# Optimization experiments

Measured on AMD Instinct MI355X. Metric: run time of the kernel, lower is better.

## Reference

```python
import jax, jax.numpy as jnp
import numpy as np
from jax import lax

B, T, D, H = 4, 2048, 1024, 8
DK = D // H        # head qk dim (expand_k=1.0) = 128
DV = 2 * D // H    # head v dim (expand_v=2.0) = 256
C = 64             # retention chunk size


def setup_inputs() -> dict:
    key = jax.random.key(0)
    ks = jax.random.split(key, 7)
    s = 0.02
    return {
        "x": jax.random.normal(ks[0], (B, T, D), jnp.float32),
        "Wq": jax.random.normal(ks[1], (D, H * DK), jnp.float32) * s,
        "Wk": jax.random.normal(ks[2], (D, H * DK), jnp.float32) * s,
        "Wv": jax.random.normal(ks[3], (D, H * DV), jnp.float32) * s,
        "Wg": jax.random.normal(ks[4], (D, H * DV), jnp.float32) * s,
        "Wo": jax.random.normal(ks[5], (H * DV, D), jnp.float32) * s,
        "norm_w": jnp.ones((DV,), jnp.float32),
    }


def _rope(x):
    # x: [B,T,H,DK]; GPT-NeoX style (non-interleaved) rotary, base 10000
    half = DK // 2
    inv = 1.0 / (10000.0 ** (jnp.arange(0, DK, 2, dtype=jnp.float32) / DK))
    f = jnp.arange(T, dtype=jnp.float32)[:, None] * inv[None, :]  # [T, half]
    cos = jnp.cos(f)[None, :, None, :]
    sin = jnp.sin(f)[None, :, None, :]
    x1, x2 = x[..., :half], x[..., half:]
    return jnp.concatenate([x1 * cos - x2 * sin, x2 * cos + x1 * sin], axis=-1)


def _retention(q, k, v):
    # chunked decay-gated linear attention (RetNet retention)
    # q,k: [B,T,H,DK], v: [B,T,H,DV]; recurrence S_t = g*S_{t-1} + k_t^T v_t, o_t = q_t S_t
    N = T // C
    gamma = 1.0 - 2.0 ** (-5.0 - jnp.arange(H, dtype=jnp.float32))  # [H] per-head decay
    i = jnp.arange(C, dtype=jnp.float32)
    expo = i[:, None] - i[None, :]                                   # [C,C]
    M = jnp.where(expo >= 0, gamma[:, None, None] ** expo[None], 0.0)  # [H,C,C] intra-chunk decay mask
    dec_q = gamma[:, None] ** (i + 1.0)        # [H,C] decay of state seen by q_i
    dec_k = gamma[:, None] ** (C - 1.0 - i)    # [H,C] decay of k_j into end-of-chunk state
    gC = gamma ** C

    def to_chunks(t):
        return t.reshape(B, N, C, H, -1).transpose(1, 0, 3, 2, 4)  # [N,B,H,C,d]

    qs, kcs, vcs = to_chunks(q), to_chunks(k), to_chunks(v)

    def step(S, inp):
        qc, kc, vc = inp  # [B,H,C,DK],[B,H,C,DK],[B,H,C,DV]
        attn = jnp.einsum('bhid,bhjd->bhij', qc, kc) * M[None]
        o_intra = jnp.einsum('bhij,bhje->bhie', attn, vc)
        o_inter = jnp.einsum('bhid,bhde->bhie', qc, S) * dec_q[None, :, :, None]
        kv = jnp.einsum('bhjd,bhje->bhde', kc * dec_k[None, :, :, None], vc)
        S_new = gC[None, :, None, None] * S + kv
        return S_new, o_intra + o_inter

    S0 = jnp.zeros((B, H, DK, DV), q.dtype)
    _, os_ = lax.scan(step, S0, (qs, kcs, vcs))  # os_: [N,B,H,C,DV]
    return os_.transpose(1, 0, 3, 2, 4).reshape(B, T, H, DV)


def reference(x, Wq, Wk, Wv, Wg, Wo, norm_w):
    q = (x @ Wq).reshape(B, T, H, DK)
    k = (x @ Wk).reshape(B, T, H, DK)
    v = (x @ Wv).reshape(B, T, H, DV)
    g = (x @ Wg).reshape(B, T, H, DV)
    q, k = _rope(q), _rope(k)
    q = q * (DK ** -0.5)
    o = _retention(q, k, v)
    # fused per-head RMSNorm + swish output gate (FusedRMSNormSwishGate)
    rms = jnp.sqrt(jnp.mean(o * o, axis=-1, keepdims=True) + 1e-5)
    o = (o / rms) * norm_w
    o = o * g * jax.nn.sigmoid(g)
    return o.reshape(B, T, H * DV) @ Wo
```

## Files before the change

### kernel.cpp

```cpp
#include <hip/hip_runtime.h>
#include <hip/hip_bf16.h>
#include <cstdint>
#include <cstddef>

using f32x4 = __attribute__((ext_vector_type(4))) float;
using s16x8 = __attribute__((ext_vector_type(8))) short;
using s16x4 = __attribute__((ext_vector_type(4))) short;

#define DEVINL __device__ __forceinline__

static constexpr int T_LEN  = 2048;
static constexpr int MROWS  = 8192;
static constexpr int NCHUNK = 32;

DEVINL float bf2f(short s){
  unsigned u = ((unsigned)(unsigned short)s) << 16;
  return __builtin_bit_cast(float, u);
}
DEVINL short f2bf(float f){
  unsigned u = __builtin_bit_cast(unsigned, f);
  u = (u + 0x7fffu + ((u >> 16) & 1u)) >> 16;
  return (short)(unsigned short)u;
}

#define GLOAD16(gp, lp) \
  __builtin_amdgcn_global_load_lds((__attribute__((address_space(1))) void*)(gp), \
                                   (__attribute__((address_space(3))) void*)(lp), 16, 0, 0)

#define MFMA16(a, b, c) __builtin_amdgcn_mfma_f32_16x16x32_bf16((a), (b), (c), 0, 0, 0)

__global__ __launch_bounds__(256) void cvt_f32_bf16(const float* __restrict__ in,
                                                    short* __restrict__ out, int n4){
  int i = blockIdx.x * 256 + threadIdx.x;
  if (i >= n4) return;
  float4 v = ((const float4*)in)[i];
  short4 o;
  o.x = f2bf(v.x); o.y = f2bf(v.y); o.z = f2bf(v.z); o.w = f2bf(v.w);
  ((short4*)out)[i] = o;
}

__global__ __launch_bounds__(256) void tr_w(const float* __restrict__ in,
                                            short* __restrict__ out, int R, int C){
  __shared__ float tile[32][33];
  int c0 = blockIdx.x * 32, r0 = blockIdx.y * 32;
  int tx = threadIdx.x, ty = threadIdx.y;
  #pragma unroll
  for (int i = 0; i < 4; ++i){
    int r = ty + i * 8;
    tile[r][tx] = in[(size_t)(r0 + r) * C + c0 + tx];
  }
  __syncthreads();
  #pragma unroll
  for (int i = 0; i < 4; ++i){
    int c = ty + i * 8;
    out[(size_t)(c0 + c) * R + r0 + tx] = f2bf(tile[tx][c]);
  }
}

__global__ __launch_bounds__(256) void tr_k_decay(const short* __restrict__ in,
                                                  short* __restrict__ out){
  __shared__ float tile[32][33];
  int c0 = blockIdx.x * 32, r0 = blockIdx.y * 32;
  int tx = threadIdx.x, ty = threadIdx.y;
  #pragma unroll
  for (int i = 0; i < 4; ++i){
    int r = ty + i * 8;
    tile[r][tx] = bf2f(in[(size_t)(r0 + r) * 1024 + c0 + tx]);
  }
  __syncthreads();
  #pragma unroll
  for (int i = 0; i < 4; ++i){
    int c  = c0 + ty + i * 8;
    int h  = c >> 7;
    float lg = log2f(1.0f - exp2f(-(float)(5 + h)));
    int srow = r0 + tx;
    int j = srow & 63;
    float dec = exp2f((float)(63 - j) * lg);
    out[(size_t)c * MROWS + srow] = f2bf(tile[tx][ty + i * 8] * dec);
  }
}

__global__ __launch_bounds__(256) void rope_table(float* __restrict__ tab){
  int i = blockIdx.x * 256 + threadIdx.x;
  int t = i >> 6, d = i & 63;
  float inv = exp2f(-(float)d * (13.287712379549449f / 64.0f));
  float f = (float)t * inv;
  float s, c;
  sincosf(f, &s, &c);
  tab[2 * i]     = c;
  tab[2 * i + 1] = s;
}

__global__ __launch_bounds__(256) void rope_inplace(short* __restrict__ qk,
                                                    const float* __restrict__ tab,
                                                    float scale, int bake){
  int idx = blockIdx.x * 256 + threadIdx.x;
  int bt  = idx >> 9, rem = idx & 511;
  int h   = rem >> 6, d = rem & 63;
  int t   = bt & (T_LEN - 1);
  float2 cs = ((const float2*)tab)[t * 64 + d];
  float mult = scale;
  if (bake){
    float lg = log2f(1.0f - exp2f(-(float)(5 + h)));
    mult *= exp2f((float)((t & 63) + 1) * lg);
  }
  size_t base = (size_t)bt * 1024 + h * 128 + d;
  float x1 = bf2f(qk[base]), x2 = bf2f(qk[base + 64]);
  qk[base]      = f2bf((x1 * cs.x - x2 * cs.y) * mult);
  qk[base + 64] = f2bf((x2 * cs.x + x1 * cs.y) * mult);
}

DEVINL void stage_half(const short* __restrict__ src, int ldk, int t, int half,
                       short* lbase, int wave, int lane){
  const int sr = lane >> 3;
  const int gc = ((lane & 7) ^ sr) * 8;
  const size_t k0 = (size_t)t * 64;
  #pragma unroll
  for (int c = 0; c < 2; ++c){
    int r0 = half * 128 + c * 64;
    GLOAD16(src + (size_t)(r0 + wave * 8 + sr) * ldk + k0 + gc,
            lbase + (r0 + wave * 8) * 64);
  }
}

DEVINL s16x8 frag64(const short* buf, int row, int ks, int lhi){
  int ch = (ks * 4 + lhi) ^ (row & 7);
  return *(const s16x8*)&buf[row * 64 + ch * 8];
}

template<int MODE>
__global__ __launch_bounds__(512, 2) void gemm256(const short* __restrict__ A,
                                                  const short* __restrict__ Bt,
                                                  void* __restrict__ o0, void* __restrict__ o1,
                                                  void* __restrict__ o2, void* __restrict__ o3,
                                                  int K, int nt){
  __shared__ alignas(16) short LBUF[65536];
  const int tid = threadIdx.x, wave = tid >> 6, lane = tid & 63;
  const int l15 = lane & 15, lhi = lane >> 4;
  const int wm = (wave >> 2) * 128, wn = (wave & 3) * 64;
  const int cpx = gridDim.x >> 3;
  const int swz = (blockIdx.x & 7) * cpx + (blockIdx.x >> 3);
  const int m0 = (swz & 31) * 256, n0 = (swz >> 5) * 256;
  const short* Ag = A + (size_t)m0 * K;
  const short* Bg = Bt + (size_t)n0 * K;
  f32x4 acc[8][4] = {};
  stage_half(Ag, K, 0, 0, LBUF,                 wave, lane);
  stage_half(Ag, K, 0, 1, LBUF,                 wave, lane);
  stage_half(Bg, K, 0, 0, LBUF + 32768,         wave, lane);
  stage_half(Bg, K, 0, 1, LBUF + 32768,         wave, lane);
  stage_half(Bg, K, 1, 0, LBUF + 32768 + 16384, wave, lane);
  stage_half(Bg, K, 1, 1, LBUF + 32768 + 16384, wave, lane);
  asm volatile("s_waitcnt vmcnt(4)" ::: "memory");
  __builtin_amdgcn_sched_barrier(0);
  __builtin_amdgcn_s_barrier();
  for (int t = 0; t < nt; ++t){
    short* Ab = LBUF + (t & 1) * 16384;
    short* Bb = LBUF + 32768 + (t & 1) * 16384;
    s16x8 bfr[2][4];
    #pragma unroll
    for (int q = 0; q < 4; ++q){
      if (q == 0){
        #pragma unroll
        for (int ks = 0; ks < 2; ++ks)
          #pragma unroll
          for (int nf = 0; nf < 4; ++nf)
            bfr[ks][nf] = frag64(Bb, wn + nf * 16 + l15, ks, lhi);
      }
      s16x8 af[2][2];
      #pragma unroll
      for (int i = 0; i < 2; ++i)
        #pragma unroll
        for (int ks = 0; ks < 2; ++ks)
          af[i][ks] = frag64(Ab, wm + (2 * q + i) * 16 + l15, ks, lhi);
      if (q == 0 && t + 1 < nt) stage_half(Ag, K, t + 1, 0, LBUF + ((t + 1) & 1) * 16384, wave, lane);
      if (q == 1 && t + 1 < nt) stage_half(Ag, K, t + 1, 1, LBUF + ((t + 1) & 1) * 16384, wave, lane);
      if (q == 2 && t + 2 < nt) stage_half(Bg, K, t + 2, 0, LBUF + 32768 + (t & 1) * 16384, wave, lane);
      if (q == 3 && t + 2 < nt) stage_half(Bg, K, t + 2, 1, LBUF + 32768 + (t & 1) * 16384, wave, lane);
      __builtin_amdgcn_sched_barrier(0);
      __builtin_amdgcn_s_barrier();
      asm volatile("s_waitcnt lgkmcnt(0)" ::: "memory");
      __builtin_amdgcn_sched_barrier(0);
      __builtin_amdgcn_s_setprio(1);
      #pragma unroll
      for (int i = 0; i < 2; ++i)
        #pragma unroll
        for (int nf = 0; nf < 4; ++nf)
          #pragma unroll
          for (int ks = 0; ks < 2; ++ks)
            acc[2 * q + i][nf] = MFMA16(af[i][ks], bfr[ks][nf], acc[2 * q + i][nf]);
      __builtin_amdgcn_s_setprio(0);
      if (q == 3){
        if (t < nt - 2)       asm volatile("s_waitcnt vmcnt(4)" ::: "memory");
        else if (t == nt - 2) asm volatile("s_waitcnt vmcnt(0)" ::: "memory");
        __builtin_amdgcn_sched_barrier(0);
      }
      __builtin_amdgcn_s_barrier();
    }
  }
  if (MODE == 2){
    float* dst = (float*)o0;
    #pragma unroll
    for (int mf = 0; mf < 8; ++mf){
      int rb = m0 + wm + mf * 16 + 4 * lhi;
      #pragma unroll
      for (int nf = 0; nf < 4; ++nf){
        int col = n0 + wn + nf * 16 + l15;
        #pragma unroll
        for (int r = 0; r < 4; ++r) dst[(size_t)(rb + r) * 1024 + col] = acc[mf][nf][r];
      }
    }
  } else {
    if (n0 < 2048){
      short* dst = (short*)(n0 < 1024 ? o0 : o1);
      int cb = (n0 & 1023) + wn;
      #pragma unroll
      for (int mf = 0; mf < 8; ++mf){
        int rb = m0 + wm + mf * 16 + 4 * lhi;
        #pragma unroll
        for (int nf = 0; nf < 4; ++nf){
          int col = cb + nf * 16 + l15;
          #pragma unroll
          for (int r = 0; r < 4; ++r) dst[(size_t)(rb + r) * 1024 + col] = f2bf(acc[mf][nf][r]);
        }
      }
    } else if (n0 < 4096){
      short* dst = (short*)o2;
      #pragma unroll
      for (int mf = 0; mf < 8; ++mf){
        int rb = m0 + wm + mf * 16 + 4 * lhi;
        #pragma unroll
        for (int nf = 0; nf < 4; ++nf){
          int e = (n0 - 2048) + wn + nf * 16 + l15;
          s16x4 pk;
          #pragma unroll
          for (int r = 0; r < 4; ++r) pk[r] = f2bf(acc[mf][nf][r]);
          *(s16x4*)&dst[(size_t)e * MROWS + rb] = pk;
        }
      }
    } else {
      short* dst = (short*)o3;
      int cb = (n0 - 4096) + wn;
      #pragma unroll
      for (int mf = 0; mf < 8; ++mf){
        int rb = m0 + wm + mf * 16 + 4 * lhi;
        #pragma unroll
        for (int nf = 0; nf < 4; ++nf){
          int col = cb + nf * 16 + l15;
          #pragma unroll
          for (int r = 0; r < 4; ++r) dst[(size_t)(rb + r) * 2048 + col] = f2bf(acc[mf][nf][r]);
        }
      }
    }
  }
}

__global__ __launch_bounds__(256) void ret_scan(const short* __restrict__ kT,
                                                const short* __restrict__ vT,
                                                short* __restrict__ ST){
  __shared__ alignas(16) short kbuf[3][4096];
  __shared__ alignas(16) short vbuf[3][4096];
  const int tid = threadIdx.x, wave = tid >> 6, lane = tid & 63;
  const int db = blockIdx.x & 1, eb = blockIdx.x >> 1;
  const int h = blockIdx.y, b = blockIdx.z;
  const int d0 = db * 64, e0 = eb * 64;
  const float lg = log2f(1.0f - exp2f(-(float)(5 + h)));
  const float gC = exp2f(64.0f * lg);
  f32x4 Sacc[4] = {};
  const int srow = wave * 8 + (lane >> 3);
  const int sc   = lane & 7;

  auto STAGE = [&](int n, int buf){
    size_t rowbase = (size_t)(b * T_LEN + n * 64);
    #pragma unroll
    for (int c = 0; c < 2; ++c){
      int r = c * 32 + srow;
      int gc = sc ^ (r & 7);
      GLOAD16(kT + (size_t)(h * 128 + d0 + r) * MROWS + rowbase + gc * 8,
              &kbuf[buf][c * 2048 + wave * 512]);
    }
    #pragma unroll
    for (int c = 0; c < 2; ++c){
      int r = c * 32 + srow;
      int gc = sc ^ (r & 7);
      GLOAD16(vT + (size_t)(h * 256 + e0 + r) * MROWS + rowbase + gc * 8,
              &vbuf[buf][c * 2048 + wave * 512]);
    }
  };

  STAGE(0, 0);
  STAGE(1, 1);
  for (int n = 0; n < NCHUNK; ++n){
    const int buf = n % 3;
    if (n + 2 < NCHUNK) STAGE(n + 2, (n + 2) % 3);
    if (n > 0){
      size_t stb = (((size_t)n * 4 + b) * 8 + h) * 32768;
      int dbase = d0 + 16 * wave + 4 * (lane >> 4);
      #pragma unroll
      for (int nf = 0; nf < 4; ++nf){
        int e = e0 + nf * 16 + (lane & 15);
        s16x4 pk;
        #pragma unroll
        for (int r = 0; r < 4; ++r) pk[r] = f2bf(Sacc[nf][r]);
        *(s16x4*)&ST[stb + (size_t)e * 128 + dbase] = pk;
      }
    }
    if (n == 0)       asm volatile("s_waitcnt vmcnt(8)"  ::: "memory");
    else if (n < 30)  asm volatile("s_waitcnt vmcnt(12)" ::: "memory");
    else if (n == 30) asm volatile("s_waitcnt vmcnt(8)"  ::: "memory");
    else              asm volatile("s_waitcnt vmcnt(4)"  ::: "memory");
    __builtin_amdgcn_s_barrier();
    __builtin_amdgcn_sched_barrier(0);
    #pragma unroll
    for (int nf = 0; nf < 4; ++nf)
      #pragma unroll
      for (int r = 0; r < 4; ++r) Sacc[nf][r] *= gC;
    #pragma unroll
    for (int ks = 0; ks < 2; ++ks){
      int d = 16 * wave + (lane & 15);
      int chA = (ks * 4 + (lane >> 4)) ^ (d & 7);
      s16x8 af = *(const s16x8*)&kbuf[buf][d * 64 + chA * 8];
      #pragma unroll
      for (int nf = 0; nf < 4; ++nf){
        int e = nf * 16 + (lane & 15);
        int chB = (ks * 4 + (lane >> 4)) ^ (e & 7);
        s16x8 bv = *(const s16x8*)&vbuf[buf][e * 64 + chB * 8];
        Sacc[nf] = MFMA16(af, bv, Sacc[nf]);
      }
    }
    __builtin_amdgcn_s_barrier();
    __builtin_amdgcn_sched_barrier(0);
  }
}

__global__ __launch_bounds__(256, 2) void ret_fused(const short* __restrict__ q,
                                                    const short* __restrict__ k,
                                                    const short* __restrict__ vT,
                                                    const short* __restrict__ ST,
                                                    const short* __restrict__ g,
                                                    const float* __restrict__ nw,
                                                    short* __restrict__ y){
  __shared__ alignas(16) short GS[16384];
  __shared__ alignas(16) float SS[256];
  __shared__ alignas(16) short XS[16896];
  short* PS = XS;
  short* YT = XS;
  const int tid = threadIdx.x, wave = tid >> 6, lane = tid & 63;
  const int l15 = lane & 15, lhi = lane >> 4;
  const int n = blockIdx.x, h = blockIdx.y, b = blockIdx.z;
  const size_t rowbase = (size_t)(b * T_LEN + n * 64);
  {
    int row = wave * 2 + (lane >> 5), sc32 = lane & 31;
    #pragma unroll
    for (int c = 0; c < 8; ++c){
      int r = c * 8 + row;
      GLOAD16(g + (rowbase + r) * 2048 + h * 256 + sc32 * 8, &GS[c * 2048 + wave * 512]);
    }
  }
  s16x8 Qf[4][4];
  #pragma unroll
  for (int rf = 0; rf < 4; ++rf)
    #pragma unroll
    for (int ks = 0; ks < 4; ++ks)
      Qf[rf][ks] = *(const s16x8*)&q[(rowbase + rf * 16 + l15) * 1024 + h * 128 + ks * 32 + lhi * 8];
  s16x8 Kf[4];
  #pragma unroll
  for (int ks = 0; ks < 4; ++ks)
    Kf[ks] = *(const s16x8*)&k[(rowbase + wave * 16 + l15) * 1024 + h * 128 + ks * 32 + lhi * 8];
  f32x4 accP[4] = {};
  #pragma unroll
  for (int ks = 0; ks < 4; ++ks)
    #pragma unroll
    for (int nf = 0; nf < 4; ++nf)
      accP[nf] = MFMA16(Kf[ks], Qf[nf][ks], accP[nf]);
  const float lg = log2f(1.0f - exp2f(-(float)(5 + h)));
  {
    int jb = wave * 16 + 4 * lhi;
    float dj[4];
    #pragma unroll
    for (int r = 0; r < 4; ++r) dj[r] = exp2f(-(float)(jb + r + 1) * lg);
    #pragma unroll
    for (int nf = 0; nf < 4; ++nf){
      int i = nf * 16 + l15;
      s16x4 pk;
      #pragma unroll
      for (int r = 0; r < 4; ++r)
        pk[r] = f2bf((i >= jb + r) ? accP[nf][r] * dj[r] : 0.0f);
      *(s16x4*)&PS[i * 72 + jb] = pk;
    }
  }
  f32x4 acc[4][4] = {};
  if (n){
    size_t stb = (((size_t)n * 4 + b) * 8 + h) * 32768;
    #pragma unroll
    for (int ks = 0; ks < 4; ++ks){
      s16x8 Sf[4];
      #pragma unroll
      for (int nf = 0; nf < 4; ++nf){
        int e = wave * 64 + nf * 16 + l15;
        Sf[nf] = *(const s16x8*)&ST[stb + (size_t)e * 128 + ks * 32 + lhi * 8];
      }
      #pragma unroll
      for (int mf = 0; mf < 4; ++mf)
        #pragma unroll
        for (int nf = 0; nf < 4; ++nf)
          acc[mf][nf] = MFMA16(Qf[mf][ks], Sf[nf], acc[mf][nf]);
    }
  }
  s16x8 Vf[2][4];
  #pragma unroll
  for (int ks2 = 0; ks2 < 2; ++ks2)
    #pragma unroll
    for (int nf = 0; nf < 4; ++nf){
      int e = wave * 64 + nf * 16 + l15;
      Vf[ks2][nf] = *(const s16x8*)&vT[(size_t)(h * 256 + e) * MROWS + rowbase + ks2 * 32 + lhi * 8];
    }
  __syncthreads();
  #pragma unroll
  for (int ks2 = 0; ks2 < 2; ++ks2){
    s16x8 Pf[4];
    #pragma unroll
    for (int mf = 0; mf < 4; ++mf)
      Pf[mf] = *(const s16x8*)&PS[(mf * 16 + l15) * 72 + ks2 * 32 + lhi * 8];
    #pragma unroll
    for (int mf = 0; mf < 4; ++mf)
      #pragma unroll
      for (int nf = 0; nf < 4; ++nf)
        acc[mf][nf] = MFMA16(Pf[mf], Vf[ks2][nf], acc[mf][nf]);
  }
  float ssp[4][4];
  #pragma unroll
  for (int mf = 0; mf < 4; ++mf)
    #pragma unroll
    for (int r = 0; r < 4; ++r){
      float s = 0.f;
      #pragma unroll
      for (int nf = 0; nf < 4; ++nf) s += acc[mf][nf][r] * acc[mf][nf][r];
      #pragma unroll
      for (int off = 8; off >= 1; off >>= 1) s += __shfl_xor(s, off, 64);
      ssp[mf][r] = s;
    }
  if (l15 == 0){
    #pragma unroll
    for (int mf = 0; mf < 4; ++mf)
      #pragma unroll
      for (int r = 0; r < 4; ++r){
        int row = mf * 16 + 4 * lhi + r;
        SS[row * 4 + wave] = ssp[mf][r];
      }
  }
  __syncthreads();
  #pragma unroll
  for (int mf = 0; mf < 4; ++mf){
    float rr[4];
    #pragma unroll
    for (int r = 0; r < 4; ++r){
      int row = mf * 16 + 4 * lhi + r;
      f32x4 s4 = *(const f32x4*)&SS[row * 4];
      float tot = s4[0] + s4[1] + s4[2] + s4[3];
      rr[r] = __builtin_amdgcn_rsqf(tot * (1.0f / 256.0f) + 1e-5f);
    }
    #pragma unroll
    for (int nf = 0; nf < 4; ++nf){
      int e = wave * 64 + nf * 16 + l15;
      float nwe = nw[e];
      #pragma unroll
      for (int r = 0; r < 4; ++r){
        int row = mf * 16 + 4 * lhi + r;
        float gf = bf2f(GS[row * 256 + e]);
        float sig = __builtin_amdgcn_rcpf(1.0f + exp2f(gf * -1.4426950408889634f));
        YT[row * 264 + e] = f2bf(acc[mf][nf][r] * rr[r] * nwe * gf * sig);
      }
    }
  }
  __syncthreads();
  #pragma unroll
  for (int it = 0; it < 8; ++it){
    int flat = it * 2048 + tid * 8;
    int row = flat >> 8, e = flat & 255;
    s16x8 v = *(const s16x8*)&YT[row * 264 + e];
    *(s16x8*)&y[(rowbase + row) * 2048 + h * 256 + e] = v;
  }
}

extern "C" void kernel_launch(void* const* d_in, const int* in_sizes, int n_in,
                              void* d_out, int out_size, void* d_ws, size_t ws_size,
                              hipStream_t stream){
  const float* x  = (const float*)d_in[0];
  const float* Wq = (const float*)d_in[1];
  const float* Wk = (const float*)d_in[2];
  const float* Wv = (const float*)d_in[3];
  const float* Wg = (const float*)d_in[4];
  const float* Wo = (const float*)d_in[5];
  const float* nw = (const float*)d_in[6];
  float* out = (float*)d_out;

  char* w = (char*)d_ws;
  short* xb  = (short*)w;               w += (size_t)8192 * 1024 * 2;
  short* WT  = (short*)w;               w += (size_t)6144 * 1024 * 2;
  short* kTt = (short*)w;               w += (size_t)1024 * 8192 * 2;
  short* qb  = (short*)w;               w += (size_t)8192 * 1024 * 2;
  short* kb  = (short*)w;               w += (size_t)8192 * 1024 * 2;
  short* vT  = (short*)w;               w += (size_t)2048 * 8192 * 2;
  short* gb  = (short*)w;               w += (size_t)8192 * 2048 * 2;
  short* STb = (short*)w;               w += (size_t)32 * 4 * 8 * 32768 * 2;
  short* WoT = (short*)w;               w += (size_t)1024 * 2048 * 2;
  short* yb  = (short*)d_ws;
  float* tab = (float*)STb;

  cvt_f32_bf16<<<8192, 256, 0, stream>>>(x, xb, 8192 * 1024 / 4);
  dim3 tb(32, 8);
  tr_w<<<dim3(32, 32), tb, 0, stream>>>(Wq, WT,                       1024, 1024);
  tr_w<<<dim3(32, 32), tb, 0, stream>>>(Wk, WT + (size_t)1024 * 1024, 1024, 1024);
  tr_w<<<dim3(64, 32), tb, 0, stream>>>(Wv, WT + (size_t)2048 * 1024, 1024, 2048);
  tr_w<<<dim3(64, 32), tb, 0, stream>>>(Wg, WT + (size_t)4096 * 1024, 1024, 2048);
  tr_w<<<dim3(32, 64), tb, 0, stream>>>(Wo, WoT,                      2048, 1024);
  rope_table<<<512, 256, 0, stream>>>(tab);

  gemm256<3><<<768, 512, 0, stream>>>(xb, WT, qb, kb, vT, gb, 1024, 16);

  rope_inplace<<<16384, 256, 0, stream>>>(qb, tab, 0.08838834764831845f, 1);
  rope_inplace<<<16384, 256, 0, stream>>>(kb, tab, 1.0f, 0);
  tr_k_decay<<<dim3(32, 256), tb, 0, stream>>>(kb, kTt);

  ret_scan <<<dim3(8, 8, 4),  256, 0, stream>>>(kTt, vT, STb);
  ret_fused<<<dim3(32, 8, 4), 256, 0, stream>>>(qb, kb, vT, STb, gb, nw, yb);

  gemm256<2><<<128, 512, 0, stream>>>(yb, WoT, out, nullptr, nullptr, nullptr, 2048, 32);
}
```

Baseline: 307.1 us.

## Triple-buffer A tiles, use BM=128 for output GEMM, remap XCD tile order

The GEMM now triple-buffers the A tile so A is prefetched two k-steps ahead, matching the B prefetch, instead of one step ahead. The output projection GEMM uses a 128-row M tile and 256 blocks instead of 128 blocks, which fills more CUs on the small output GEMM. Block-to-tile mapping now groups M tiles per XCD, so each XCD reuses the same B panel. The cost is more LDS per block (about 160KB for BM=256), which may limit occupancy below the declared two blocks per CU.

Measured after the change: 288.3 us. -6.1%, faster.

```diff
diff --git a/kernel.cpp b/kernel.cpp
--- a/kernel.cpp
+++ b/kernel.cpp
@@ -110,19 +110,6 @@
   qk[base + 64] = f2bf((x2 * cs.x + x1 * cs.y) * mult);
 }
 
-DEVINL void stage_half(const short* __restrict__ src, int ldk, int t, int half,
-                       short* lbase, int wave, int lane){
-  const int sr = lane >> 3;
-  const int gc = ((lane & 7) ^ sr) * 8;
-  const size_t k0 = (size_t)t * 64;
-  #pragma unroll
-  for (int c = 0; c < 2; ++c){
-    int r0 = half * 128 + c * 64;
-    GLOAD16(src + (size_t)(r0 + wave * 8 + sr) * ldk + k0 + gc,
-            lbase + (r0 + wave * 8) * 64);
-  }
-}
-
 DEVINL s16x8 frag64(const short* buf, int row, int ks, int lhi){
   int ch = (ks * 4 + lhi) ^ (row & 7);
   return *(const s16x8*)&buf[row * 64 + ch * 8];
@@ -133,29 +120,60 @@
                                                   const short* __restrict__ Bt,
                                                   void* __restrict__ o0, void* __restrict__ o1,
                                                   void* __restrict__ o2, void* __restrict__ o3,
-                                                  int K, int nt){
-  __shared__ alignas(16) short LBUF[65536];
+                                                  int K, int nt, int NT){
+  constexpr int BM   = (MODE == 2 ? 128 : 256);
+  constexpr int ABUF = BM * 64;
+  constexpr int MF   = BM / 32;
+  constexpr int RPP  = MF / 4;
+  __shared__ alignas(16) short LBUF[3 * ABUF + 2 * 16384];
+  short* const BB = LBUF + 3 * ABUF;
   const int tid = threadIdx.x, wave = tid >> 6, lane = tid & 63;
   const int l15 = lane & 15, lhi = lane >> 4;
-  const int wm = (wave >> 2) * 128, wn = (wave & 3) * 64;
-  const int cpx = gridDim.x >> 3;
-  const int swz = (blockIdx.x & 7) * cpx + (blockIdx.x >> 3);
-  const int m0 = (swz & 31) * 256, n0 = (swz >> 5) * 256;
+  const int wm = (wave >> 2) * (BM / 2), wn = (wave & 3) * 64;
+  const int MG  = (gridDim.x >> 3) / NT;
+  const int xcd = blockIdx.x & 7, idx = blockIdx.x >> 3;
+  const int mi  = idx % MG, nn = idx / MG;
+  const int m0  = (xcd * MG + mi) * BM, n0 = nn * 256;
   const short* Ag = A + (size_t)m0 * K;
   const short* Bg = Bt + (size_t)n0 * K;
-  f32x4 acc[8][4] = {};
-  stage_half(Ag, K, 0, 0, LBUF,                 wave, lane);
-  stage_half(Ag, K, 0, 1, LBUF,                 wave, lane);
-  stage_half(Bg, K, 0, 0, LBUF + 32768,         wave, lane);
-  stage_half(Bg, K, 0, 1, LBUF + 32768,         wave, lane);
-  stage_half(Bg, K, 1, 0, LBUF + 32768 + 16384, wave, lane);
-  stage_half(Bg, K, 1, 1, LBUF + 32768 + 16384, wave, lane);
-  asm volatile("s_waitcnt vmcnt(4)" ::: "memory");
+  const int sr = lane >> 3;
+  const int gc = ((lane & 7) ^ sr) * 8;
+  f32x4 acc[MF][4] = {};
+
+  auto stageA = [&](int t, int half){
+    short* lb = LBUF + (t % 3) * ABUF;
+    size_t k0 = (size_t)t * 64;
+    if constexpr (BM == 256){
+      #pragma unroll
+      for (int c = 0; c < 2; ++c){
+        int r0 = half * 128 + c * 64;
+        GLOAD16(Ag + (size_t)(r0 + wave * 8 + sr) * K + k0 + gc, lb + (r0 + wave * 8) * 64);
+      }
+    } else {
+      int r0 = half * 64;
+      GLOAD16(Ag + (size_t)(r0 + wave * 8 + sr) * K + k0 + gc, lb + (r0 + wave * 8) * 64);
+    }
+  };
+  auto stageB = [&](int t, int half){
+    short* lb = BB + (t & 1) * 16384;
+    size_t k0 = (size_t)t * 64;
+    #pragma unroll
+    for (int c = 0; c < 2; ++c){
+      int r0 = half * 128 + c * 64;
+      GLOAD16(Bg + (size_t)(r0 + wave * 8 + sr) * K + k0 + gc, lb + (r0 + wave * 8) * 64);
+    }
+  };
+
+  stageA(0, 0); stageA(0, 1); stageB(0, 0); stageB(0, 1);
+  stageA(1, 0); stageA(1, 1); stageB(1, 0); stageB(1, 1);
+  if constexpr (BM == 256) asm volatile("s_waitcnt vmcnt(8)" ::: "memory");
+  else                     asm volatile("s_waitcnt vmcnt(6)" ::: "memory");
   __builtin_amdgcn_sched_barrier(0);
   __builtin_amdgcn_s_barrier();
+
   for (int t = 0; t < nt; ++t){
-    short* Ab = LBUF + (t & 1) * 16384;
-    short* Bb = LBUF + 32768 + (t & 1) * 16384;
+    const short* Ab = LBUF + (t % 3) * ABUF;
+    const short* Bb = BB + (t & 1) * 16384;
     s16x8 bfr[2][4];
     #pragma unroll
     for (int q = 0; q < 4; ++q){
@@ -166,32 +184,38 @@
           for (int nf = 0; nf < 4; ++nf)
             bfr[ks][nf] = frag64(Bb, wn + nf * 16 + l15, ks, lhi);
       }
-      s16x8 af[2][2];
-      #pragma unroll
-      for (int i = 0; i < 2; ++i)
+      s16x8 af[RPP][2];
+      #pragma unroll
+      for (int i = 0; i < RPP; ++i)
         #pragma unroll
         for (int ks = 0; ks < 2; ++ks)
-          af[i][ks] = frag64(Ab, wm + (2 * q + i) * 16 + l15, ks, lhi);
-      if (q == 0 && t + 1 < nt) stage_half(Ag, K, t + 1, 0, LBUF + ((t + 1) & 1) * 16384, wave, lane);
-      if (q == 1 && t + 1 < nt) stage_half(Ag, K, t + 1, 1, LBUF + ((t + 1) & 1) * 16384, wave, lane);
-      if (q == 2 && t + 2 < nt) stage_half(Bg, K, t + 2, 0, LBUF + 32768 + (t & 1) * 16384, wave, lane);
-      if (q == 3 && t + 2 < nt) stage_half(Bg, K, t + 2, 1, LBUF + 32768 + (t & 1) * 16384, wave, lane);
+          af[i][ks] = frag64(Ab, wm + (RPP * q + i) * 16 + l15, ks, lhi);
+      if (t + 2 < nt){
+        if (q == 0) stageA(t + 2, 0);
+        if (q == 1) stageA(t + 2, 1);
+        if (q == 2) stageB(t + 2, 0);
+        if (q == 3) stageB(t + 2, 1);
+      }
       __builtin_amdgcn_sched_barrier(0);
       __builtin_amdgcn_s_barrier();
       asm volatile("s_waitcnt lgkmcnt(0)" ::: "memory");
       __builtin_amdgcn_sched_barrier(0);
       __builtin_amdgcn_s_setprio(1);
       #pragma unroll
-      for (int i = 0; i < 2; ++i)
+      for (int i = 0; i < RPP; ++i)
         #pragma unroll
         for (int nf = 0; nf < 4; ++nf)
           #pragma unroll
           for (int ks = 0; ks < 2; ++ks)
-            acc[2 * q + i][nf] = MFMA16(af[i][ks], bfr[ks][nf], acc[2 * q + i][nf]);
+            acc[RPP * q + i][nf] = MFMA16(af[i][ks], bfr[ks][nf], acc[RPP * q + i][nf]);
       __builtin_amdgcn_s_setprio(0);
       if (q == 3){
-        if (t < nt - 2)       asm volatile("s_waitcnt vmcnt(4)" ::: "memory");
-        else if (t == nt - 2) asm volatile("s_waitcnt vmcnt(0)" ::: "memory");
+        if (t < nt - 2){
+          if constexpr (BM == 256) asm volatile("s_waitcnt vmcnt(8)" ::: "memory");
+          else                     asm volatile("s_waitcnt vmcnt(6)" ::: "memory");
+        } else if (t == nt - 2){
+          asm volatile("s_waitcnt vmcnt(0)" ::: "memory");
+        }
         __builtin_amdgcn_sched_barrier(0);
       }
       __builtin_amdgcn_s_barrier();
@@ -200,7 +224,7 @@
   if (MODE == 2){
     float* dst = (float*)o0;
     #pragma unroll
-    for (int mf = 0; mf < 8; ++mf){
+    for (int mf = 0; mf < MF; ++mf){
       int rb = m0 + wm + mf * 16 + 4 * lhi;
       #pragma unroll
       for (int nf = 0; nf < 4; ++nf){
@@ -214,7 +238,7 @@
       short* dst = (short*)(n0 < 1024 ? o0 : o1);
       int cb = (n0 & 1023) + wn;
       #pragma unroll
-      for (int mf = 0; mf < 8; ++mf){
+      for (int mf = 0; mf < MF; ++mf){
         int rb = m0 + wm + mf * 16 + 4 * lhi;
         #pragma unroll
         for (int nf = 0; nf < 4; ++nf){
@@ -226,7 +250,7 @@
     } else if (n0 < 4096){
       short* dst = (short*)o2;
       #pragma unroll
-      for (int mf = 0; mf < 8; ++mf){
+      for (int mf = 0; mf < MF; ++mf){
         int rb = m0 + wm + mf * 16 + 4 * lhi;
         #pragma unroll
         for (int nf = 0; nf < 4; ++nf){
@@ -241,7 +265,7 @@
       short* dst = (short*)o3;
       int cb = (n0 - 4096) + wn;
       #pragma unroll
-      for (int mf = 0; mf < 8; ++mf){
+      for (int mf = 0; mf < MF; ++mf){
         int rb = m0 + wm + mf * 16 + 4 * lhi;
         #pragma unroll
         for (int nf = 0; nf < 4; ++nf){
@@ -516,7 +540,7 @@
   tr_w<<<dim3(32, 64), tb, 0, stream>>>(Wo, WoT,                      2048, 1024);
   rope_table<<<512, 256, 0, stream>>>(tab);
 
-  gemm256<3><<<768, 512, 0, stream>>>(xb, WT, qb, kb, vT, gb, 1024, 16);
+  gemm256<3><<<768, 512, 0, stream>>>(xb, WT, qb, kb, vT, gb, 1024, 16, 24);
 
   rope_inplace<<<16384, 256, 0, stream>>>(qb, tab, 0.08838834764831845f, 1);
   rope_inplace<<<16384, 256, 0, stream>>>(kb, tab, 1.0f, 0);
@@ -525,5 +549,5 @@
   ret_scan <<<dim3(8, 8, 4),  256, 0, stream>>>(kTt, vT, STb);
   ret_fused<<<dim3(32, 8, 4), 256, 0, stream>>>(qb, kb, vT, STb, gb, nw, yb);
 
-  gemm256<2><<<128, 512, 0, stream>>>(yb, WoT, out, nullptr, nullptr, nullptr, 2048, 32);
-}
+  gemm256<2><<<256, 512, 0, stream>>>(yb, WoT, out, nullptr, nullptr, nullptr, 2048, 32, 4);
+}
```
